# Optimization experiments

Measured on AMD Instinct MI355X. Metric: run time of the kernel, lower is better.

The kernel has to match this reference:

```python
import jax, jax.numpy as jnp
import numpy as np
import math


def setup_inputs() -> dict:
    key = jax.random.key(0)
    ks = jax.random.split(key, 5)
    B, S, H = 4, 2048, 512
    scale = 1.0 / math.sqrt(H)
    return {
        "input_seq_rep": jax.random.normal(ks[0], (B, S, H), dtype=jnp.float32),
        "Wk": jax.random.normal(ks[1], (H, H), dtype=jnp.float32) * scale,
        "bk": jax.random.normal(ks[2], (H,), dtype=jnp.float32) * 0.01,
        "Wq": jax.random.normal(ks[3], (H, H), dtype=jnp.float32) * scale,
        "bq": jax.random.normal(ks[4], (H,), dtype=jnp.float32) * 0.01,
        "k_mul": 64,
    }


def reference(input_seq_rep, Wk, bk, Wq, bq, k_mul):
    B, S, H = input_seq_rep.shape
    x = jax.nn.relu(input_seq_rep)
    # torch Linear: y = x @ W.T + b
    k = jnp.einsum("bsh,oh->bso", x, Wk) + bk  # key (also used as value)
    q = jnp.einsum("bsh,oh->bso", x, Wq) + bq

    # local causal band mask: max(0, i - k_mul) <= j <= i
    i = jnp.arange(S)[:, None]
    j = jnp.arange(S)[None, :]
    mask = (j >= jnp.maximum(i - k_mul, 0)) & (j <= i)  # [S, S] bool

    scores = jnp.einsum("bqh,bkh->bqk", q, k) / jnp.sqrt(jnp.asarray(H, q.dtype))
    scores = jnp.where(mask[None, :, :], scores, jnp.asarray(-1e9, scores.dtype))
    attn = jax.nn.softmax(scores, axis=-1)  # [B, S, S]
    out = jnp.einsum("bqk,bkh->bqh", attn, k)  # value == key
    return out, attn
```

## Files before the change

kernel.cpp:

```cpp
#include <hip/hip_runtime.h>
#include <hip/hip_bf16.h>
#include <float.h>
#include <math.h>


typedef __attribute__((ext_vector_type(4))) float f32x4;
typedef __attribute__((ext_vector_type(8))) short short8;
typedef __attribute__((ext_vector_type(4))) short short4v;

#define TM 128
#define TN 128
#define TK 64

#define QBLK 16
#define KW 96
#define SCP 100
#define PPAD 104

static __device__ __forceinline__ short f2bf(float f) {
    __hip_bfloat16 h = __float2bfloat16(f);
    return *reinterpret_cast<short*>(&h);
}

__global__ __launch_bounds__(256) void gemm_mfma_relu_bias_bf16(
    const float* __restrict__ A,
    const float* __restrict__ Wq, const float* __restrict__ bq, short* __restrict__ Cq,
    const float* __restrict__ Wk, const float* __restrict__ bk, short* __restrict__ Ck,
    short* __restrict__ CkT,
    int M, int N, int K, int sshift)
{
    const float* W    = blockIdx.z ? Wk : Wq;
    const float* bias = blockIdx.z ? bk : bq;
    short*       C    = blockIdx.z ? Ck : Cq;

    __shared__ __align__(16) short lds[TM * TN];
    short* As = lds;
    short* Bs = lds + TM * TK;

    const int tid  = threadIdx.x;
    const int lane = tid & 63;
    const int wave = tid >> 6;
    const int wr   = (wave >> 1) * 64;
    const int wc   = (wave & 1) * 64;
    const int m0   = blockIdx.x * TM;
    const int n0   = blockIdx.y * TN;

    const int lr = lane & 15;
    const int lk = (lane >> 4) * 8;

    f32x4 acc[4][4];
    #pragma unroll
    for (int m = 0; m < 4; ++m)
        #pragma unroll
        for (int n = 0; n < 4; ++n)
            #pragma unroll
            for (int r = 0; r < 4; ++r) acc[m][n][r] = 0.f;

    for (int k0 = 0; k0 < K; k0 += TK) {
        #pragma unroll
        for (int i = 0; i < 8; ++i) {
            int f   = tid + (i << 8);
            int row = f >> 4;
            int cq  = (f & 15) << 2;
            int sidx = row * TK + (cq ^ ((row & 7) << 3));
            float4 va = *(const float4*)&A[(size_t)(m0 + row) * K + k0 + cq];
            short4v sa;
            sa.x = f2bf(fmaxf(va.x, 0.f));
            sa.y = f2bf(fmaxf(va.y, 0.f));
            sa.z = f2bf(fmaxf(va.z, 0.f));
            sa.w = f2bf(fmaxf(va.w, 0.f));
            *(short4v*)&As[sidx] = sa;
            float4 vb = *(const float4*)&W[(size_t)(n0 + row) * K + k0 + cq];
            short4v sb;
            sb.x = f2bf(vb.x);
            sb.y = f2bf(vb.y);
            sb.z = f2bf(vb.z);
            sb.w = f2bf(vb.w);
            *(short4v*)&Bs[sidx] = sb;
        }
        __syncthreads();

        #pragma unroll
        for (int kk = 0; kk < 2; ++kk) {
            short8 af[4], bf[4];
            #pragma unroll
            for (int m = 0; m < 4; ++m) {
                int r = wr + m * 16 + lr;
                af[m] = *(const short8*)&As[r * TK + ((kk * 32 + lk) ^ ((r & 7) << 3))];
            }
            #pragma unroll
            for (int n = 0; n < 4; ++n) {
                int r = wc + n * 16 + lr;
                bf[n] = *(const short8*)&Bs[r * TK + ((kk * 32 + lk) ^ ((r & 7) << 3))];
            }
            #pragma unroll
            for (int m = 0; m < 4; ++m)
                #pragma unroll
                for (int n = 0; n < 4; ++n)
                    acc[m][n] = __builtin_amdgcn_mfma_f32_16x16x32_bf16(
                        af[m], bf[n], acc[m][n], 0, 0, 0);
        }
        __syncthreads();
    }

    float bv[4];
    #pragma unroll
    for (int n = 0; n < 4; ++n) bv[n] = bias[n0 + wc + n * 16 + lr];
    const int cr = (lane >> 4) * 4;

    #pragma unroll
    for (int m = 0; m < 4; ++m)
        #pragma unroll
        for (int n = 0; n < 4; ++n) {
            int col = wc + n * 16 + lr;
            #pragma unroll
            for (int r = 0; r < 4; ++r) {
                int row = wr + m * 16 + cr + r;
                lds[row * TN + (col ^ ((row & 7) << 3))] = f2bf(acc[m][n][r] + bv[n]);
            }
        }
    __syncthreads();
    #pragma unroll
    for (int i = 0; i < 8; ++i) {
        int idx = tid + (i << 8);
        int m = idx >> 4, n8 = (idx & 15) << 3;
        short8 v = *(const short8*)&lds[m * TN + (n8 ^ ((m & 7) << 3))];
        *(short8*)&C[(size_t)(m0 + m) * N + n0 + n8] = v;
    }

    if (blockIdx.z) {
        __syncthreads();
        #pragma unroll
        for (int m = 0; m < 4; ++m)
            #pragma unroll
            for (int n = 0; n < 4; ++n) {
                int col = wc + n * 16 + lr;
                #pragma unroll
                for (int r = 0; r < 4; ++r) {
                    int row = wr + m * 16 + cr + r;
                    lds[col * TM + (row ^ ((col & 7) << 3))] = f2bf(acc[m][n][r] + bv[n]);
                }
            }
        __syncthreads();
        const int smask = (1 << sshift) - 1;
        #pragma unroll
        for (int i = 0; i < 8; ++i) {
            int idx = tid + (i << 8);
            int n = idx >> 4, m8 = (idx & 15) << 3;
            short8 v = *(const short8*)&lds[n * TM + (m8 ^ ((n & 7) << 3))];
            int gm = m0 + m8;
            int gb = gm >> sshift, s = gm & smask;
            *(short8*)&CkT[((size_t)gb * N + (n0 + n)) * (size_t)(smask + 1) + s] = v;
        }
    }
}

__global__ __launch_bounds__(512) void band_attn_mfma(
    const short* __restrict__ qbf, const short* __restrict__ kbf,
    const short* __restrict__ kT, const int* __restrict__ kmul_p,
    float* __restrict__ out, float* __restrict__ attn,
    int S, int H, float scale)
{
    __shared__ float sc[QBLK][SCP];
    __shared__ short pl[QBLK][PPAD];

    int bx = blockIdx.x;
    int tile = bx;
    if ((gridDim.x & 7) == 0) {
        int chunk = gridDim.x >> 3;
        tile = (bx & 7) * chunk + (bx >> 3);
    }

    const int i0  = tile * QBLK;
    const int b   = blockIdx.y;
    const int tid = threadIdx.x;
    const int lane = tid & 63;
    const int w    = tid >> 6;
    const int km   = kmul_p[0];
    const int jbase = max(i0 - (KW - QBLK), 0);

    const int lr = lane & 15;
    const int lk = (lane >> 4) * 8;
    const int fr = (lane >> 4) * 4;

    const short* qb = qbf + ((size_t)b * S + i0) * H;
    const short* kb = kbf + ((size_t)b * S + jbase) * H;
    if (w < 6) {
        f32x4 sacc;
        #pragma unroll
        for (int r = 0; r < 4; ++r) sacc[r] = 0.f;
        #pragma unroll
        for (int ks = 0; ks < 16; ++ks) {
            int hoff = ks * 32 + lk;
            short8 qa = *(const short8*)(qb + (size_t)lr * H + hoff);
            short8 kf = *(const short8*)(kb + (size_t)(w * 16 + lr) * H + hoff);
            sacc = __builtin_amdgcn_mfma_f32_16x16x32_bf16(qa, kf, sacc, 0, 0, 0);
        }
        int key = w * 16 + lr;
        int kg  = jbase + key;
        #pragma unroll
        for (int r = 0; r < 4; ++r) {
            int q = fr + r;
            int irow = i0 + q;
            bool ok = (kg <= irow) && (kg + km >= irow);
            sc[q][key] = ok ? sacc[r] * scale : -1e30f;
        }
    }
    __syncthreads();

    if (tid < 256) {
        int r = tid >> 4;
        int t = tid & 15;
        float v[6];
        #pragma unroll
        for (int c = 0; c < 6; ++c) v[c] = sc[r][t * 6 + c];
        float mx = -FLT_MAX;
        #pragma unroll
        for (int c = 0; c < 6; ++c) mx = fmaxf(mx, v[c]);
        mx = fmaxf(mx, __shfl_xor(mx, 1, 64));
        mx = fmaxf(mx, __shfl_xor(mx, 2, 64));
        mx = fmaxf(mx, __shfl_xor(mx, 4, 64));
        mx = fmaxf(mx, __shfl_xor(mx, 8, 64));
        float e[6], s = 0.f;
        #pragma unroll
        for (int c = 0; c < 6; ++c) { e[c] = __expf(v[c] - mx); s += e[c]; }
        s += __shfl_xor(s, 1, 64);
        s += __shfl_xor(s, 2, 64);
        s += __shfl_xor(s, 4, 64);
        s += __shfl_xor(s, 8, 64);
        float inv = __frcp_rn(s);
        #pragma unroll
        for (int c = 0; c < 6; ++c) {
            float p = e[c] * inv;
            sc[r][t * 6 + c] = p;
            pl[r][t * 6 + c] = f2bf(p);
        }
    }
    __syncthreads();

    short8 pa[3];
    #pragma unroll
    for (int ks = 0; ks < 3; ++ks)
        pa[ks] = *(const short8*)&pl[lr][ks * 32 + lk];

    const short* ktb = kT + (size_t)b * H * S;
    float* obase = out + ((size_t)b * S + i0) * H;
    #pragma unroll
    for (int nf = 0; nf < 4; ++nf) {
        int h = w * 64 + nf * 16 + lr;
        f32x4 oacc;
        #pragma unroll
        for (int r = 0; r < 4; ++r) oacc[r] = 0.f;
        #pragma unroll
        for (int ks = 0; ks < 3; ++ks) {
            short8 kf = *(const short8*)(ktb + (size_t)h * S + jbase + ks * 32 + lk);
            oacc = __builtin_amdgcn_mfma_f32_16x16x32_bf16(pa[ks], kf, oacc, 0, 0, 0);
        }
        #pragma unroll
        for (int r = 0; r < 4; ++r) {
            int q = fr + r;
            __builtin_nontemporal_store(oacc[r], obase + (size_t)q * H + h);
        }
    }

    float* abase = attn + ((size_t)b * S + i0) * (size_t)S;
    const int col = tid * 4;
    #pragma unroll 4
    for (int r = 0; r < QBLK; ++r) {
        f32x4 o;
        #pragma unroll
        for (int j = 0; j < 4; ++j) {
            int rel = col + j - jbase;
            o[j] = ((unsigned)rel < (unsigned)KW) ? sc[r][rel] : 0.f;
        }
        __builtin_nontemporal_store(o, (f32x4*)(abase + (size_t)r * S + col));
    }
}

extern "C" void kernel_launch(void* const* d_in, const int* in_sizes, int n_in,
                              void* d_out, int out_size, void* d_ws, size_t ws_size,
                              hipStream_t stream)
{
    const float* x  = (const float*)d_in[0];
    const float* Wk = (const float*)d_in[1];
    const float* bk = (const float*)d_in[2];
    const float* Wq = (const float*)d_in[3];
    const float* bq = (const float*)d_in[4];
    const int*   km = (const int*)d_in[5];

    const int H = in_sizes[2];
    const long long BS = (long long)in_sizes[0] / H;
    const long long S = ((long long)out_size - (long long)in_sizes[0]) / BS;
    const int B = (int)(BS / S);
    int sshift = 0;
    while ((1LL << sshift) < S) ++sshift;

    short* kT  = (short*)d_ws;
    short* qbf = kT + (size_t)B * H * S;
    short* kbf = qbf + (size_t)BS * H;

    dim3 gg((unsigned)(BS / TM), (unsigned)(H / TN), 2);
    gemm_mfma_relu_bias_bf16<<<gg, 256, 0, stream>>>(
        x, Wq, bq, qbf, Wk, bk, kbf, kT, (int)BS, H, H, sshift);

    float* outp  = (float*)d_out;
    float* attnp = outp + (size_t)BS * H;
    const float scale = 1.0f / sqrtf((float)H);

    dim3 ag((unsigned)(S / QBLK), (unsigned)B);
    band_attn_mfma<<<ag, 512, 0, stream>>>(qbf, kbf, kT, km, outp, attnp,
                                           (int)S, H, scale);
}
```

Baseline: 56.19 us.

## Zero-fill attention matrix inside projection GEMM; write only band in attention kernel

New measurement: 49.54 us. 1.13x faster.

```diff
diff --git a/kernel.cpp b/kernel.cpp
--- a/kernel.cpp
+++ b/kernel.cpp
@@ -26,7 +26,7 @@
     const float* __restrict__ A,
     const float* __restrict__ Wq, const float* __restrict__ bq, short* __restrict__ Cq,
     const float* __restrict__ Wk, const float* __restrict__ bk, short* __restrict__ Ck,
-    short* __restrict__ CkT,
+    short* __restrict__ CkT, float* __restrict__ attnz, long long zPerBlk4,
     int M, int N, int K, int sshift)
 {
     const float* W    = blockIdx.z ? Wk : Wq;
@@ -44,6 +44,13 @@
     const int wc   = (wave & 1) * 64;
     const int m0   = blockIdx.x * TM;
     const int n0   = blockIdx.y * TN;
+
+    const int blkLin = blockIdx.x + gridDim.x * (blockIdx.y + gridDim.y * blockIdx.z);
+    f32x4* zp = (f32x4*)attnz;
+    const size_t zbase = (size_t)blkLin * (size_t)zPerBlk4;
+    const int nsteps = K / TK;
+    const int perStep = (int)(zPerBlk4 / ((long long)nsteps * 256));
+    const f32x4 z4 = {0.f, 0.f, 0.f, 0.f};
 
     const int lr = lane & 15;
     const int lk = (lane >> 4) * 8;
@@ -100,6 +107,13 @@
                     acc[m][n] = __builtin_amdgcn_mfma_f32_16x16x32_bf16(
                         af[m], bf[n], acc[m][n], 0, 0, 0);
         }
+
+        {
+            int s = k0 / TK;
+            size_t off = zbase + (size_t)s * perStep * 256 + tid;
+            for (int j = 0; j < perStep; ++j)
+                zp[off + (size_t)j * 256] = z4;
+        }
         __syncthreads();
     }
 
@@ -263,17 +277,13 @@
         }
     }
 
-    float* abase = attn + ((size_t)b * S + i0) * (size_t)S;
-    const int col = tid * 4;
-    #pragma unroll 4
-    for (int r = 0; r < QBLK; ++r) {
+    if (tid < (KW / 4) * QBLK) {
+        int r = tid / (KW / 4);
+        int c = tid % (KW / 4);
         f32x4 o;
         #pragma unroll
-        for (int j = 0; j < 4; ++j) {
-            int rel = col + j - jbase;
-            o[j] = ((unsigned)rel < (unsigned)KW) ? sc[r][rel] : 0.f;
-        }
-        __builtin_nontemporal_store(o, (f32x4*)(abase + (size_t)r * S + col));
+        for (int j = 0; j < 4; ++j) o[j] = sc[r][c * 4 + j];
+        *(f32x4*)(attn + ((size_t)b * S + i0 + r) * (size_t)S + jbase + c * 4) = o;
     }
 }
 
@@ -299,12 +309,17 @@
     short* qbf = kT + (size_t)B * H * S;
     short* kbf = qbf + (size_t)BS * H;
 
-    dim3 gg((unsigned)(BS / TM), (unsigned)(H / TN), 2);
-    gemm_mfma_relu_bias_bf16<<<gg, 256, 0, stream>>>(
-        x, Wq, bq, qbf, Wk, bk, kbf, kT, (int)BS, H, H, sshift);
-
     float* outp  = (float*)d_out;
     float* attnp = outp + (size_t)BS * H;
+
+    dim3 gg((unsigned)(BS / TM), (unsigned)(H / TN), 2);
+    const long long nblk = (long long)gg.x * gg.y * 2;
+    const long long zPerBlk4 = ((long long)B * S * S / 4) / nblk;
+
+    gemm_mfma_relu_bias_bf16<<<gg, 256, 0, stream>>>(
+        x, Wq, bq, qbf, Wk, bk, kbf, kT, attnp, zPerBlk4,
+        (int)BS, H, H, sshift);
+
     const float scale = 1.0f / sqrtf((float)H);
 
     dim3 ag((unsigned)(S / QBLK), (unsigned)B);
```
